# Kernel tuning notes

Hardware: AMD Instinct MI355X
Metric: run time of the kernel (lower is better)

Reference implementation:

```python
import jax, jax.numpy as jnp
import numpy as np

GRID_SIZE = 5
SPLINE_ORDER = 3
LN_EPS = 1e-5


def make_grid(dtype=jnp.float32):
    # efficient-kan default grid over [-1, 1], extended by spline_order on each side
    h = 2.0 / GRID_SIZE
    return jnp.arange(-SPLINE_ORDER, GRID_SIZE + SPLINE_ORDER + 1, dtype=dtype) * h - 1.0  # (12,)


def b_splines(x, grid):
    # Cox-de Boor recursion. x: (B, Cin) -> bases: (B, Cin, GRID_SIZE+SPLINE_ORDER)
    xe = x[..., None]  # (B, Cin, 1)
    bases = ((xe >= grid[:-1]) & (xe < grid[1:])).astype(x.dtype)  # order-0, (B,Cin,11)
    for k in range(1, SPLINE_ORDER + 1):
        left = (xe - grid[: -(k + 1)]) / (grid[k:-1] - grid[: -(k + 1)]) * bases[..., :-1]
        right = (grid[k + 1:] - xe) / (grid[k + 1:] - grid[1:-k]) * bases[..., 1:]
        bases = left + right
    return bases


def setup_inputs() -> dict:
    key = jax.random.key(0)
    k0, k1, k2, k3 = jax.random.split(key, 4)
    B, T, C, O = 512, 197, 768, 1000
    G = GRID_SIZE + SPLINE_ORDER
    x = jax.random.normal(k0, (B, T, C), jnp.float32)
    ln_weight = jnp.ones((T, C), jnp.float32)
    ln_bias = jnp.zeros((T, C), jnp.float32)
    base_weight = jax.random.normal(k1, (O, C), jnp.float32) * (1.0 / np.sqrt(C))
    spline_weight = jax.random.normal(k2, (O, C, G), jnp.float32) * 0.1
    spline_scaler = 1.0 + 0.1 * jax.random.normal(k3, (O, C), jnp.float32)
    return {"x": x, "ln_weight": ln_weight, "ln_bias": ln_bias,
            "base_weight": base_weight, "spline_weight": spline_weight,
            "spline_scaler": spline_scaler}


def reference(x, ln_weight, ln_bias, base_weight, spline_weight, spline_scaler):
    # LayerNorm over the last two dims [n_tokens, n_channel]
    mean = x.mean(axis=(1, 2), keepdims=True)
    var = x.var(axis=(1, 2), keepdims=True)  # biased, as in torch LayerNorm
    xn = (x - mean) * jax.lax.rsqrt(var + LN_EPS) * ln_weight + ln_bias
    # permute -> AdaptiveAvgPool1d(1) -> squeeze == mean over token axis
    pooled = xn.mean(axis=1)  # (B, C)
    # KANLinear: base path (SiLU + linear) + spline path
    base_out = jax.nn.silu(pooled) @ base_weight.T  # (B, O)
    grid = make_grid(pooled.dtype)
    splines = b_splines(pooled, grid)  # (B, C, 8)
    scaled_w = spline_weight * spline_scaler[..., None]  # (O, C, 8)
    spline_out = jnp.einsum('bcg,ocg->bo', splines, scaled_w)
    return base_out + spline_out
```

## Files before the change

### kernel.cpp

```cpp
#include <hip/hip_runtime.h>
#include <hip/hip_bf16.h>
#include <cstdint>

#define B_SZ 512
#define T_SZ 197
#define C_SZ 768
#define O_SZ 1000
#define K_SZ (C_SZ + C_SZ * 8)
#define NPAD 1024
#define LN_EPS 1e-5f

typedef __bf16 bf16;
typedef __bf16 bf16x4 __attribute__((ext_vector_type(4)));
typedef __bf16 bf16x8 __attribute__((ext_vector_type(8)));
typedef float  f32x4  __attribute__((ext_vector_type(4)));

__global__ __launch_bounds__(256) void k0_wbmean(
    const float* __restrict__ lnw, const float* __restrict__ lnb,
    float* __restrict__ wmean, float* __restrict__ bmean)
{
    int c = blockIdx.x * 256 + threadIdx.x;
    if (c >= C_SZ) return;
    float sw = 0.f, sb = 0.f;
    for (int t = 0; t < T_SZ; ++t) {
        sw += lnw[t * C_SZ + c];
        sb += lnb[t * C_SZ + c];
    }
    const float invT = 1.0f / T_SZ;
    wmean[c] = sw * invT;
    bmean[c] = sb * invT;
}

__global__ __launch_bounds__(256) void k2_prep_w(
    const float* __restrict__ bw, const float* __restrict__ sw,
    const float* __restrict__ ss, bf16* __restrict__ Wc)
{
    const int o = blockIdx.x;
    const int tid = threadIdx.x;
    bf16* row = Wc + (size_t)o * K_SZ;
    if (o >= O_SZ) {
        bf16x8 z = {};
        for (int i = tid; i < K_SZ / 8; i += 256)
            *(bf16x8*)(row + i * 8) = z;
        return;
    }
    for (int c = tid; c < C_SZ; c += 256)
        row[c] = (bf16)bw[(size_t)o * C_SZ + c];
    for (int c = tid; c < C_SZ; c += 256) {
        float sc = ss[(size_t)o * C_SZ + c];
        const float4* swp = (const float4*)(sw + ((size_t)o * C_SZ + c) * 8);
        float4 w0 = swp[0], w1 = swp[1];
        bf16x8 v;
        v[0] = (bf16)(w0.x * sc); v[1] = (bf16)(w0.y * sc);
        v[2] = (bf16)(w0.z * sc); v[3] = (bf16)(w0.w * sc);
        v[4] = (bf16)(w1.x * sc); v[5] = (bf16)(w1.y * sc);
        v[6] = (bf16)(w1.z * sc); v[7] = (bf16)(w1.w * sc);
        *(bf16x8*)(row + C_SZ + (size_t)c * 8) = v;
    }
}

__global__ __launch_bounds__(384) void k1_pool_feat(
    const float* __restrict__ x, const float* __restrict__ lnw,
    const float* __restrict__ wmean, const float* __restrict__ bmean,
    bf16* __restrict__ Act)
{
    const int b   = blockIdx.x;
    const int tid = threadIdx.x;
    const int u   = tid % 192;
    const int rg  = tid / 192;

    const float4* X4 = (const float4*)(x + (size_t)b * T_SZ * C_SZ);
    const float4* W4 = (const float4*)lnw;

    float4 a4 = make_float4(0.f, 0.f, 0.f, 0.f);
    float s = 0.f, s2 = 0.f;
    for (int r = rg; r < T_SZ; r += 2) {
        float4 xv = X4[r * 192 + u];
        float4 wv = W4[r * 192 + u];
        a4.x += wv.x * xv.x; a4.y += wv.y * xv.y;
        a4.z += wv.z * xv.z; a4.w += wv.w * xv.w;
        s  += xv.x + xv.y + xv.z + xv.w;
        s2 += xv.x * xv.x + xv.y * xv.y + xv.z * xv.z + xv.w * xv.w;
    }
    for (int off = 32; off > 0; off >>= 1) {
        s  += __shfl_down(s,  off, 64);
        s2 += __shfl_down(s2, off, 64);
    }
    __shared__ float red_s[6], red_s2[6];
    __shared__ float4 aShare[192];
    __shared__ float stats[2];
    const int wave = tid >> 6, lane = tid & 63;
    if (lane == 0) { red_s[wave] = s; red_s2[wave] = s2; }
    if (rg == 1) aShare[u] = a4;
    __syncthreads();
    if (tid == 0) {
        float S = 0.f, S2 = 0.f;
        for (int i = 0; i < 6; ++i) { S += red_s[i]; S2 += red_s2[i]; }
        const float invN = 1.0f / (float)(T_SZ * C_SZ);
        float mean = S * invN;
        float var  = S2 * invN - mean * mean;
        stats[0] = mean;
        stats[1] = rsqrtf(var + LN_EPS);
    }
    __syncthreads();
    if (rg == 0) {
        const float mean = stats[0], rstd = stats[1];
        float4 ao = aShare[u];
        a4.x += ao.x; a4.y += ao.y; a4.z += ao.z; a4.w += ao.w;
        const float invT = 1.0f / T_SZ;
        float p[4];
        bf16x4 basev;
        const float av[4] = { a4.x, a4.y, a4.z, a4.w };
        #pragma unroll
        for (int j = 0; j < 4; ++j) {
            int c = 4 * u + j;
            float pv = rstd * (av[j] * invT - mean * wmean[c]) + bmean[c];
            p[j] = pv;
            float si = pv / (1.f + expf(-pv));
            basev[j] = (bf16)si;
        }
        *(bf16x4*)(Act + (size_t)b * K_SZ + 4 * u) = basev;
        #pragma unroll
        for (int j = 0; j < 4; ++j) {
            float pv = p[j];
            float bas[11];
            #pragma unroll
            for (int i = 0; i < 11; ++i) {
                float g0 = (i - 3) * 0.4f - 1.0f;
                float g1 = (i - 2) * 0.4f - 1.0f;
                bas[i] = (pv >= g0 && pv < g1) ? 1.0f : 0.0f;
            }
            #pragma unroll
            for (int k = 1; k <= 3; ++k) {
                #pragma unroll
                for (int i = 0; i + k < 11; ++i) {
                    float gi   = (i - 3) * 0.4f - 1.0f;
                    float gik  = (i + k - 3) * 0.4f - 1.0f;
                    float gik1 = (i + k - 2) * 0.4f - 1.0f;
                    float gi1  = (i - 2) * 0.4f - 1.0f;
                    float left  = (pv - gi) / (gik - gi) * bas[i];
                    float right = (gik1 - pv) / (gik1 - gi1) * bas[i + 1];
                    bas[i] = left + right;
                }
            }
            bf16x8 sv;
            #pragma unroll
            for (int g = 0; g < 8; ++g) sv[g] = (bf16)bas[g];
            *(bf16x8*)(Act + (size_t)b * K_SZ + C_SZ + (size_t)(4 * u + j) * 8) = sv;
        }
    }
}

__global__ __launch_bounds__(256) void k3_gemm(
    const bf16* __restrict__ Act, const bf16* __restrict__ Wc,
    float* __restrict__ Out)
{
    __shared__ __align__(16) bf16 As[64][72];
    __shared__ __align__(16) bf16 Bs[64][72];
    const int tid  = threadIdx.x;
    const int bm   = blockIdx.x & 7;
    const int bn   = blockIdx.x >> 3;
    const int m0   = bm * 64, n0 = bn * 64;
    const int wave = tid >> 6, lane = tid & 63;
    const int wr   = (wave >> 1) * 32, wc = (wave & 1) * 32;
    const int lr   = lane & 15, lk = (lane >> 4) * 8;

    f32x4 acc[2][2] = {};
    const int r0 = tid >> 3,          c0 = (tid & 7) * 8;
    const int r1 = (256 + tid) >> 3,  c1 = c0;

    for (int k0 = 0; k0 < K_SZ; k0 += 64) {
        uint4 a0 = *(const uint4*)(Act + (size_t)(m0 + r0) * K_SZ + k0 + c0);
        uint4 a1 = *(const uint4*)(Act + (size_t)(m0 + r1) * K_SZ + k0 + c1);
        uint4 b0 = *(const uint4*)(Wc  + (size_t)(n0 + r0) * K_SZ + k0 + c0);
        uint4 b1 = *(const uint4*)(Wc  + (size_t)(n0 + r1) * K_SZ + k0 + c1);
        *(uint4*)(&As[r0][c0]) = a0;
        *(uint4*)(&As[r1][c1]) = a1;
        *(uint4*)(&Bs[r0][c0]) = b0;
        *(uint4*)(&Bs[r1][c1]) = b1;
        __syncthreads();
        #pragma unroll
        for (int kk = 0; kk < 64; kk += 32) {
            bf16x8 af[2], bfr[2];
            #pragma unroll
            for (int mi = 0; mi < 2; ++mi)
                af[mi] = *(const bf16x8*)(&As[wr + mi * 16 + lr][kk + lk]);
            #pragma unroll
            for (int ni = 0; ni < 2; ++ni)
                bfr[ni] = *(const bf16x8*)(&Bs[wc + ni * 16 + lr][kk + lk]);
            #pragma unroll
            for (int mi = 0; mi < 2; ++mi)
                #pragma unroll
                for (int ni = 0; ni < 2; ++ni)
                    acc[mi][ni] = __builtin_amdgcn_mfma_f32_16x16x32_bf16(
                        af[mi], bfr[ni], acc[mi][ni], 0, 0, 0);
        }
        __syncthreads();
    }
    #pragma unroll
    for (int mi = 0; mi < 2; ++mi)
        #pragma unroll
        for (int ni = 0; ni < 2; ++ni) {
            int col = n0 + wc + ni * 16 + lr;
            if (col < O_SZ) {
                #pragma unroll
                for (int j = 0; j < 4; ++j) {
                    int rowi = m0 + wr + mi * 16 + (lane >> 4) * 4 + j;
                    Out[(size_t)rowi * O_SZ + col] = acc[mi][ni][j];
                }
            }
        }
}

extern "C" void kernel_launch(void* const* d_in, const int* in_sizes, int n_in,
                              void* d_out, int out_size, void* d_ws, size_t ws_size,
                              hipStream_t stream)
{
    const float* x   = (const float*)d_in[0];
    const float* lnw = (const float*)d_in[1];
    const float* lnb = (const float*)d_in[2];
    const float* bw  = (const float*)d_in[3];
    const float* sw  = (const float*)d_in[4];
    const float* ss  = (const float*)d_in[5];
    float* Out = (float*)d_out;

    char* ws = (char*)d_ws;
    float* wmean = (float*)ws;
    float* bmean = wmean + C_SZ;
    bf16*  Act   = (bf16*)(ws + 8192);
    bf16*  Wcat  = (bf16*)(ws + 8192 + (size_t)B_SZ * K_SZ * 2);

    k0_wbmean<<<3, 256, 0, stream>>>(lnw, lnb, wmean, bmean);
    k2_prep_w<<<NPAD, 256, 0, stream>>>(bw, sw, ss, Wcat);
    k1_pool_feat<<<B_SZ, 384, 0, stream>>>(x, lnw, wmean, bmean, Act);
    k3_gemm<<<128, 256, 0, stream>>>(Act, Wcat, Out);
}
```

Measured before the change: 581.2 us.

## Split GEMM K dimension in two with atomic accumulation and parallelize LN-weight mean

The GEMM now launches 256 blocks instead of 128. Each output tile is computed by two blocks covering halves of K, and the partial sums are combined with atomic float adds into an output that a new kernel zeroes first. Separately, the LN weight/bias mean kernel spreads its token loop over 8 thread groups and 24 blocks, reducing through shared memory. The aim is better CU occupancy on the GEMM and on the tiny mean kernel, at the cost of atomic traffic, an extra zeroing launch and non-deterministic summation order.

```diff
diff --git a/kernel.cpp b/kernel.cpp
--- a/kernel.cpp
+++ b/kernel.cpp
@@ -19,16 +19,32 @@
     const float* __restrict__ lnw, const float* __restrict__ lnb,
     float* __restrict__ wmean, float* __restrict__ bmean)
 {
-    int c = blockIdx.x * 256 + threadIdx.x;
-    if (c >= C_SZ) return;
+    const int tid  = threadIdx.x;
+    const int cl   = tid & 31;
+    const int c    = blockIdx.x * 32 + cl;
+    const int tsub = tid >> 5;
     float sw = 0.f, sb = 0.f;
-    for (int t = 0; t < T_SZ; ++t) {
+    for (int t = tsub; t < T_SZ; t += 8) {
         sw += lnw[t * C_SZ + c];
         sb += lnb[t * C_SZ + c];
     }
-    const float invT = 1.0f / T_SZ;
-    wmean[c] = sw * invT;
-    bmean[c] = sb * invT;
+    __shared__ float rs[8][32], rb[8][32];
+    rs[tsub][cl] = sw;
+    rb[tsub][cl] = sb;
+    __syncthreads();
+    if (tsub == 0) {
+        float SW = 0.f, SB = 0.f;
+        #pragma unroll
+        for (int i = 0; i < 8; ++i) { SW += rs[i][cl]; SB += rb[i][cl]; }
+        const float invT = 1.0f / T_SZ;
+        wmean[c] = SW * invT;
+        bmean[c] = SB * invT;
+    }
+}
+
+__global__ __launch_bounds__(256) void kz_zero(float4* __restrict__ out)
+{
+    out[blockIdx.x * 256 + threadIdx.x] = make_float4(0.f, 0.f, 0.f, 0.f);
 }
 
 __global__ __launch_bounds__(256) void k2_prep_w(
@@ -158,9 +174,12 @@
     __shared__ __align__(16) bf16 As[64][72];
     __shared__ __align__(16) bf16 Bs[64][72];
     const int tid  = threadIdx.x;
-    const int bm   = blockIdx.x & 7;
-    const int bn   = blockIdx.x >> 3;
+    const int tile = blockIdx.x & 127;
+    const int ks   = blockIdx.x >> 7;
+    const int bm   = tile & 7;
+    const int bn   = tile >> 3;
     const int m0   = bm * 64, n0 = bn * 64;
+    const int kbeg = ks * (K_SZ / 2), kend = kbeg + K_SZ / 2;
     const int wave = tid >> 6, lane = tid & 63;
     const int wr   = (wave >> 1) * 32, wc = (wave & 1) * 32;
     const int lr   = lane & 15, lk = (lane >> 4) * 8;
@@ -169,7 +188,7 @@
     const int r0 = tid >> 3,          c0 = (tid & 7) * 8;
     const int r1 = (256 + tid) >> 3,  c1 = c0;
 
-    for (int k0 = 0; k0 < K_SZ; k0 += 64) {
+    for (int k0 = kbeg; k0 < kend; k0 += 64) {
         uint4 a0 = *(const uint4*)(Act + (size_t)(m0 + r0) * K_SZ + k0 + c0);
         uint4 a1 = *(const uint4*)(Act + (size_t)(m0 + r1) * K_SZ + k0 + c1);
         uint4 b0 = *(const uint4*)(Wc  + (size_t)(n0 + r0) * K_SZ + k0 + c0);
@@ -206,7 +225,7 @@
                 #pragma unroll
                 for (int j = 0; j < 4; ++j) {
                     int rowi = m0 + wr + mi * 16 + (lane >> 4) * 4 + j;
-                    Out[(size_t)rowi * O_SZ + col] = acc[mi][ni][j];
+                    unsafeAtomicAdd(&Out[(size_t)rowi * O_SZ + col], acc[mi][ni][j]);
                 }
             }
         }
@@ -230,8 +249,9 @@
     bf16*  Act   = (bf16*)(ws + 8192);
     bf16*  Wcat  = (bf16*)(ws + 8192 + (size_t)B_SZ * K_SZ * 2);
 
-    k0_wbmean<<<3, 256, 0, stream>>>(lnw, lnb, wmean, bmean);
+    k0_wbmean<<<24, 256, 0, stream>>>(lnw, lnb, wmean, bmean);
+    kz_zero<<<500, 256, 0, stream>>>((float4*)Out);
     k2_prep_w<<<NPAD, 256, 0, stream>>>(bw, sw, ss, Wcat);
     k1_pool_feat<<<B_SZ, 384, 0, stream>>>(x, lnw, wmean, bmean, Act);
-    k3_gemm<<<128, 256, 0, stream>>>(Act, Wcat, Out);
-}
+    k3_gemm<<<256, 256, 0, stream>>>(Act, Wcat, Out);
+}
```

Result: faster. 524.1 us (-9.8%).
